# Optimization experiments

Hardware: AMD Instinct MI355X
Metric: run time of the kernel (lower is better)

## Reference

```python
import jax, jax.numpy as jnp
import numpy as np
from jax import lax

H = 64  # hidden size


def _lstm_layer(x, w_ih, w_hh, b_ih, b_hh):
    """Single LSTM layer, batch_first x: [B, T, D] -> [B, T, H].
    PyTorch gate order: i, f, g, o."""
    B = x.shape[0]
    # Precompute input projections for all timesteps: [T, B, 4H]
    xg = jnp.einsum('btd,gd->tbg', x, w_ih) + (b_ih + b_hh)

    def step(carry, xg_t):
        h, c = carry
        gates = xg_t + h @ w_hh.T  # [B, 4H]
        i, f, g, o = jnp.split(gates, 4, axis=-1)
        i = jax.nn.sigmoid(i)
        f = jax.nn.sigmoid(f)
        g = jnp.tanh(g)
        o = jax.nn.sigmoid(o)
        c = f * c + i * g
        h = o * jnp.tanh(c)
        return (h, c), h

    h0 = jnp.zeros((B, H), dtype=x.dtype)
    c0 = jnp.zeros((B, H), dtype=x.dtype)
    (_, _), hs = lax.scan(step, (h0, c0), xg)  # hs: [T, B, H]
    return jnp.swapaxes(hs, 0, 1)  # [B, T, H]


def setup_inputs() -> dict:
    key = jax.random.key(0)
    ks = jax.random.split(key, 11)
    s = 1.0 / np.sqrt(H)  # PyTorch LSTM init scale
    x = jax.random.normal(ks[0], (8192, 168, 7), dtype=jnp.float32)
    return {
        'x': x,
        'w_ih0': jax.random.normal(ks[1], (4 * H, 7), jnp.float32) * s,
        'w_hh0': jax.random.normal(ks[2], (4 * H, H), jnp.float32) * s,
        'b_ih0': jax.random.normal(ks[3], (4 * H,), jnp.float32) * s,
        'b_hh0': jax.random.normal(ks[4], (4 * H,), jnp.float32) * s,
        'w_ih1': jax.random.normal(ks[5], (4 * H, H), jnp.float32) * s,
        'w_hh1': jax.random.normal(ks[6], (4 * H, H), jnp.float32) * s,
        'b_ih1': jax.random.normal(ks[7], (4 * H,), jnp.float32) * s,
        'b_hh1': jax.random.normal(ks[8], (4 * H,), jnp.float32) * s,
        'fc_w': jax.random.normal(ks[9], (4, H), jnp.float32) * s,
        'fc_b': jax.random.normal(ks[10], (4,), jnp.float32) * s,
    }


def reference(x, w_ih0, w_hh0, b_ih0, b_hh0, w_ih1, w_hh1, b_ih1, b_hh1, fc_w, fc_b):
    h1 = _lstm_layer(x, w_ih0, w_hh0, b_ih0, b_hh0)   # [B, T, H]
    h2 = _lstm_layer(h1, w_ih1, w_hh1, b_ih1, b_hh1)  # [B, T, H]
    last = h2[:, -1, :]                               # dropout is identity in eval
    return last @ fc_w.T + fc_b                       # [B, 4]
```

## Files before the change

kernel.cpp:

```cpp
#include <hip/hip_runtime.h>

#define TT 168
#define HH 64
#define DD 7
#define NS 16
#define BB 8192
#define CH 8
#define NTH 1024

typedef float f32x2 __attribute__((ext_vector_type(2)));
typedef float f32x4 __attribute__((ext_vector_type(4)));
typedef _Float16 f16x8 __attribute__((ext_vector_type(8)));

#define MFMA16F(A, B, C) __builtin_amdgcn_mfma_f32_16x16x32_f16((A), (B), (C), 0, 0, 0)

__device__ __forceinline__ f16x8 pack8(f32x4 a, f32x4 b) {
    f16x8 r;
#pragma unroll
    for (int e = 0; e < 4; ++e) { r[e] = (_Float16)a[e]; r[4 + e] = (_Float16)b[e]; }
    return r;
}

__device__ __forceinline__ f32x2 exp2x2(f32x2 a) {
    return (f32x2){__builtin_amdgcn_exp2f(fminf(a.x, 40.0f)),
                   __builtin_amdgcn_exp2f(fminf(a.y, 40.0f))};
}
__device__ __forceinline__ f32x2 rcpx2(f32x2 a) {
    return (f32x2){__builtin_amdgcn_rcpf(a.x), __builtin_amdgcn_rcpf(a.y)};
}

__device__ __forceinline__ void cell_pair(f32x2 si, f32x2 sf, f32x2 sg, f32x2 so,
                                          f32x2& cs, unsigned& dpk) {
    const f32x2 one = {1.0f, 1.0f};
    const f32x2 ui  = exp2x2(si);
    const f32x2 uf  = exp2x2(sf);
    const f32x2 ug  = exp2x2(sg);
    const f32x2 opf = one + uf;
    const f32x2 pig = (one + ui) * (one + ug);
    const f32x2 R1  = rcpx2(pig * opf);
    const f32x2 fv  = pig * R1;
    const f32x2 igs = (ug * 2.88539008f - (f32x2){2.88539008f, 2.88539008f}) * (opf * R1);
    cs = fv * cs + igs;
    const f32x2 uo = exp2x2(so);
    const f32x2 uc = exp2x2(cs);
    const f32x2 R2 = rcpx2((one + uo) * (one + uc));
    const f32x2 hv = (one - uc) * R2;
    asm("v_cvt_pkrtz_f16_f32 %0, %1, %2" : "=v"(dpk) : "v"(hv.x), "v"(hv.y));
}

__global__ __launch_bounds__(NTH, 8)
void weather_lstm_mfma(const float* __restrict__ x,
                       const float* __restrict__ w_ih0, const float* __restrict__ w_hh0,
                       const float* __restrict__ b_ih0, const float* __restrict__ b_hh0,
                       const float* __restrict__ w_ih1, const float* __restrict__ w_hh1,
                       const float* __restrict__ b_ih1, const float* __restrict__ b_hh1,
                       const float* __restrict__ fc_w, const float* __restrict__ fc_b,
                       float* __restrict__ out)
{
    __shared__ f16x8 xs[2][CH][4][NS];
    __shared__ __align__(16) _Float16 h1[2][NS][72];
    __shared__ __align__(16) _Float16 h2[2][NS][72];

    const int tid  = threadIdx.x;
    const int wv   = tid >> 6;
    const int u    = wv & 7;
    const int lane = tid & 63;
    const int col  = lane & 15;
    const int kg   = lane >> 4;
    const int s0   = blockIdx.x * NS;
    const int uw   = 8 * u + 2 * kg;

    for (int i = tid; i < 2 * NS * 72; i += NTH) {
        ((short*)h1)[i] = 0; ((short*)h2)[i] = 0;
    }
    {
        const f16x8 z8i = {0, 0, 0, 0, 0, 0, 0, 0};
        f16x8* xf = &xs[0][0][0][0];
        for (int i = tid; i < 2 * CH * 4 * NS; i += NTH) xf[i] = z8i;
    }
    __syncthreads();
    if (tid < CH * NS) {
        const int tloc = tid >> 4, ss = tid & 15;
        const float* px = x + ((size_t)(s0 + ss) * TT + tloc) * DD;
        f32x4 a, b;
        a[0] = px[0]; a[1] = px[1]; a[2] = px[2]; a[3] = px[3];
        b[0] = px[4]; b[1] = px[5]; b[2] = px[6]; b[3] = 1.0f;
        xs[0][tloc][0][ss] = pack8(a, b);
    }
    __syncthreads();

    const f32x4 zz = {0, 0, 0, 0};

    if (wv < 8) {
        f16x8 W0[2][2], WX[2];
#pragma unroll
        for (int t = 0; t < 2; ++t) {
            const int gsel = 2 * t + (col & 1);
            const float sc = (gsel == 2) ? -2.88539008f : -1.44269504f;
            const int row = 64 * gsel + 8 * u + (col >> 1);
#pragma unroll
            for (int kf = 0; kf < 2; ++kf) {
                const float* p = w_hh0 + (size_t)row * HH + 32 * kf + 8 * kg;
                W0[t][kf] = pack8(*(const f32x4*)p * sc, *(const f32x4*)(p + 4) * sc);
            }
            f32x4 a = {0, 0, 0, 0}, b = {0, 0, 0, 0};
            if (kg == 0) {
                const float* p = w_ih0 + (size_t)row * DD;
                a[0] = p[0]; a[1] = p[1]; a[2] = p[2]; a[3] = p[3];
                b[0] = p[4]; b[1] = p[5]; b[2] = p[6];
                b[3] = b_ih0[row] + b_hh0[row];
            }
            WX[t] = pack8(a * sc, b * sc);
        }
        f32x2 cs = {0, 0};

        const f16x8* xk = &xs[0][0][kg][col];
        const _Float16* r0 = &h1[0][col][8 * kg];
        const _Float16* r1 = r0 + NS * 72;
        unsigned* wp0 = (unsigned*)&h1[0][col][uw];
        unsigned* wp1 = (unsigned*)((_Float16*)wp0 + NS * 72);

        auto l0_step = [&](int xofs, const _Float16* r, unsigned* wr) {
            const f16x8 ax = xk[xofs];
            f32x4 aP = MFMA16F(WX[0], ax, zz);
            f32x4 aQ = MFMA16F(WX[1], ax, zz);
            f16x8 dh = *(const f16x8*)r;
            aP = MFMA16F(W0[0][0], dh, aP);
            aQ = MFMA16F(W0[1][0], dh, aQ);
            dh = *(const f16x8*)(r + 32);
            aP = MFMA16F(W0[0][1], dh, aP);
            aQ = MFMA16F(W0[1][1], dh, aQ);
            unsigned dpk;
            cell_pair((f32x2){aP[0], aP[2]}, (f32x2){aP[1], aP[3]},
                      (f32x2){aQ[0], aQ[2]}, (f32x2){aQ[1], aQ[3]}, cs, dpk);
            *wr = dpk;
        };
        auto refill = [&](int kref) {
            if (tid < CH * NS) {
                const int tloc = tid >> 4, ss = tid & 15;
                const int tg = kref + CH + tloc;
                const float* px = x + ((size_t)(s0 + ss) * TT + tg) * DD;
                f32x4 a, b;
                a[0] = px[0]; a[1] = px[1]; a[2] = px[2]; a[3] = px[3];
                b[0] = px[4]; b[1] = px[5]; b[2] = px[6]; b[3] = 1.0f;
                const int nb = ((kref >> 3) & 1) ^ 1;
                xs[nb][tloc][0][ss] = pack8(a, b);
            }
        };

        refill(0);
        l0_step(0, r1, wp0);
        __syncthreads();
        l0_step(64, r0, wp1);
        __syncthreads();

#pragma unroll 1
        for (int j = 1; j < 84; ++j) {
            const int xofs = ((2 * j) & 15) * 64;
            if ((j & 3) == 0 && j < 80) refill(2 * j);
            l0_step(xofs, r1, wp0);
            __syncthreads();
            l0_step(xofs + 64, r0, wp1);
            __syncthreads();
        }
        __syncthreads();
    } else {
        f16x8 W1[2][4];
        f32x4 bias1[2];
#pragma unroll
        for (int t = 0; t < 2; ++t) {
            const int gsel = 2 * t + (col & 1);
            const float sc = (gsel == 2) ? -2.88539008f : -1.44269504f;
            const int row = 64 * gsel + 8 * u + (col >> 1);
#pragma unroll
            for (int kf = 0; kf < 4; ++kf) {
                const float* base = (kf < 2) ? (w_ih1 + (size_t)row * HH + 32 * kf)
                                             : (w_hh1 + (size_t)row * HH + 32 * (kf - 2));
                const float* p = base + 8 * kg;
                W1[t][kf] = pack8(*(const f32x4*)p * sc, *(const f32x4*)(p + 4) * sc);
            }
#pragma unroll
            for (int e = 0; e < 4; ++e) {
                const int g2 = 2 * t + (e & 1);
                const float sce = (g2 == 2) ? -2.88539008f : -1.44269504f;
                const int br = 64 * g2 + 8 * u + 2 * kg + (e >> 1);
                bias1[t][e] = (b_ih1[br] + b_hh1[br]) * sce;
            }
        }
        f32x2 cs = {0, 0};

        const _Float16* p10 = &h1[0][col][8 * kg];
        const _Float16* p11 = p10 + NS * 72;
        const _Float16* p20 = &h2[0][col][8 * kg];
        const _Float16* p21 = p20 + NS * 72;
        unsigned* q0 = (unsigned*)&h2[0][col][uw];
        unsigned* q1 = (unsigned*)((_Float16*)q0 + NS * 72);

        auto l1_step = [&](const _Float16* h1p, const _Float16* h2p, unsigned* wr) {
            f16x8 dh = *(const f16x8*)h1p;
            f32x4 aP = MFMA16F(W1[0][0], dh, bias1[0]);
            f32x4 aQ = MFMA16F(W1[1][0], dh, bias1[1]);
            dh = *(const f16x8*)(h1p + 32);
            aP = MFMA16F(W1[0][1], dh, aP);
            aQ = MFMA16F(W1[1][1], dh, aQ);
            dh = *(const f16x8*)h2p;
            aP = MFMA16F(W1[0][2], dh, aP);
            aQ = MFMA16F(W1[1][2], dh, aQ);
            dh = *(const f16x8*)(h2p + 32);
            aP = MFMA16F(W1[0][3], dh, aP);
            aQ = MFMA16F(W1[1][3], dh, aQ);
            unsigned dpk;
            cell_pair((f32x2){aP[0], aP[2]}, (f32x2){aP[1], aP[3]},
                      (f32x2){aQ[0], aQ[2]}, (f32x2){aQ[1], aQ[3]}, cs, dpk);
            *wr = dpk;
        };

        __syncthreads();
        l1_step(p10, p21, q0);
        __syncthreads();

#pragma unroll 1
        for (int j = 1; j < 84; ++j) {
            l1_step(p11, p20, q1);
            __syncthreads();
            l1_step(p10, p21, q0);
            __syncthreads();
        }
        l1_step(p11, p20, q1);
        __syncthreads();
    }

    if (tid < NS * 4) {
        const int s = tid >> 2, k = tid & 3;
        float a = fc_b[k];
#pragma unroll
        for (int j = 0; j < HH; ++j)
            a = fmaf((float)h2[1][s][j], fc_w[k * HH + j], a);
        out[(size_t)(s0 + s) * 4 + k] = a;
    }
}

extern "C" void kernel_launch(void* const* d_in, const int* in_sizes, int n_in,
                              void* d_out, int out_size, void* d_ws, size_t ws_size,
                              hipStream_t stream) {
    const float* x     = (const float*)d_in[0];
    const float* w_ih0 = (const float*)d_in[1];
    const float* w_hh0 = (const float*)d_in[2];
    const float* b_ih0 = (const float*)d_in[3];
    const float* b_hh0 = (const float*)d_in[4];
    const float* w_ih1 = (const float*)d_in[5];
    const float* w_hh1 = (const float*)d_in[6];
    const float* b_ih1 = (const float*)d_in[7];
    const float* b_hh1 = (const float*)d_in[8];
    const float* fc_w  = (const float*)d_in[9];
    const float* fc_b  = (const float*)d_in[10];
    float* out = (float*)d_out;

    dim3 grid(BB / NS), block(NTH);
    weather_lstm_mfma<<<grid, block, 0, stream>>>(
        x, w_ih0, w_hh0, b_ih0, b_hh0,
        w_ih1, w_hh1, b_ih1, b_hh1, fc_w, fc_b, out);
}
```

Baseline: 227.1 us.

## Split LSTM steps into MFMA and cell phases, staggering layers across barriers

Each recurrent step is split into a matrix-core phase and an elementwise cell phase, separated by block barriers. The layer-0 and layer-1 wave groups are offset so that one group's MFMA phase lines up with the other group's transcendental cell phase. The aim is to let matrix-core and vector/SFU work from the two layers overlap on the CU. The cost is twice as many __syncthreads per step, and the barrier counts of the two branches must match exactly.

```diff
diff --git a/kernel.cpp b/kernel.cpp
--- a/kernel.cpp
+++ b/kernel.cpp
@@ -113,6 +113,7 @@
             WX[t] = pack8(a * sc, b * sc);
         }
         f32x2 cs = {0, 0};
+        f32x4 aP, aQ;
 
         const f16x8* xk = &xs[0][0][kg][col];
         const _Float16* r0 = &h1[0][col][8 * kg];
@@ -120,16 +121,18 @@
         unsigned* wp0 = (unsigned*)&h1[0][col][uw];
         unsigned* wp1 = (unsigned*)((_Float16*)wp0 + NS * 72);
 
-        auto l0_step = [&](int xofs, const _Float16* r, unsigned* wr) {
+        auto l0_mfma = [&](int xofs, const _Float16* r) {
             const f16x8 ax = xk[xofs];
-            f32x4 aP = MFMA16F(WX[0], ax, zz);
-            f32x4 aQ = MFMA16F(WX[1], ax, zz);
+            aP = MFMA16F(WX[0], ax, zz);
+            aQ = MFMA16F(WX[1], ax, zz);
             f16x8 dh = *(const f16x8*)r;
             aP = MFMA16F(W0[0][0], dh, aP);
             aQ = MFMA16F(W0[1][0], dh, aQ);
             dh = *(const f16x8*)(r + 32);
             aP = MFMA16F(W0[0][1], dh, aP);
             aQ = MFMA16F(W0[1][1], dh, aQ);
+        };
+        auto l0_cell = [&](unsigned* wr) {
             unsigned dpk;
             cell_pair((f32x2){aP[0], aP[2]}, (f32x2){aP[1], aP[3]},
                       (f32x2){aQ[0], aQ[2]}, (f32x2){aQ[1], aQ[3]}, cs, dpk);
@@ -149,21 +152,22 @@
         };
 
         refill(0);
-        l0_step(0, r1, wp0);
-        __syncthreads();
-        l0_step(64, r0, wp1);
-        __syncthreads();
+        l0_mfma(0, r1);        __syncthreads();
+        l0_cell(wp0);          __syncthreads();
+        l0_mfma(64, r0);       __syncthreads();
+        l0_cell(wp1);          __syncthreads();
 
 #pragma unroll 1
         for (int j = 1; j < 84; ++j) {
             const int xofs = ((2 * j) & 15) * 64;
             if ((j & 3) == 0 && j < 80) refill(2 * j);
-            l0_step(xofs, r1, wp0);
-            __syncthreads();
-            l0_step(xofs + 64, r0, wp1);
-            __syncthreads();
-        }
-        __syncthreads();
+            l0_mfma(xofs, r1);       __syncthreads();
+            l0_cell(wp0);            __syncthreads();
+            l0_mfma(xofs + 64, r0);  __syncthreads();
+            l0_cell(wp1);            __syncthreads();
+        }
+        __syncthreads(); __syncthreads();
+        __syncthreads(); __syncthreads();
     } else {
         f16x8 W1[2][4];
         f32x4 bias1[2];
@@ -188,6 +192,7 @@
             }
         }
         f32x2 cs = {0, 0};
+        f32x4 bP, bQ;
 
         const _Float16* p10 = &h1[0][col][8 * kg];
         const _Float16* p11 = p10 + NS * 72;
@@ -196,37 +201,41 @@
         unsigned* q0 = (unsigned*)&h2[0][col][uw];
         unsigned* q1 = (unsigned*)((_Float16*)q0 + NS * 72);
 
-        auto l1_step = [&](const _Float16* h1p, const _Float16* h2p, unsigned* wr) {
+        auto l1_mfma = [&](const _Float16* h1p, const _Float16* h2p) {
             f16x8 dh = *(const f16x8*)h1p;
-            f32x4 aP = MFMA16F(W1[0][0], dh, bias1[0]);
-            f32x4 aQ = MFMA16F(W1[1][0], dh, bias1[1]);
+            bP = MFMA16F(W1[0][0], dh, bias1[0]);
+            bQ = MFMA16F(W1[1][0], dh, bias1[1]);
             dh = *(const f16x8*)(h1p + 32);
-            aP = MFMA16F(W1[0][1], dh, aP);
-            aQ = MFMA16F(W1[1][1], dh, aQ);
+            bP = MFMA16F(W1[0][1], dh, bP);
+            bQ = MFMA16F(W1[1][1], dh, bQ);
             dh = *(const f16x8*)h2p;
-            aP = MFMA16F(W1[0][2], dh, aP);
-            aQ = MFMA16F(W1[1][2], dh, aQ);
+            bP = MFMA16F(W1[0][2], dh, bP);
+            bQ = MFMA16F(W1[1][2], dh, bQ);
             dh = *(const f16x8*)(h2p + 32);
-            aP = MFMA16F(W1[0][3], dh, aP);
-            aQ = MFMA16F(W1[1][3], dh, aQ);
+            bP = MFMA16F(W1[0][3], dh, bP);
+            bQ = MFMA16F(W1[1][3], dh, bQ);
+        };
+        auto l1_cell = [&](unsigned* wr) {
             unsigned dpk;
-            cell_pair((f32x2){aP[0], aP[2]}, (f32x2){aP[1], aP[3]},
-                      (f32x2){aQ[0], aQ[2]}, (f32x2){aQ[1], aQ[3]}, cs, dpk);
+            cell_pair((f32x2){bP[0], bP[2]}, (f32x2){bP[1], bP[3]},
+                      (f32x2){bQ[0], bQ[2]}, (f32x2){bQ[1], bQ[3]}, cs, dpk);
             *wr = dpk;
         };
 
+        __syncthreads(); __syncthreads();
         __syncthreads();
-        l1_step(p10, p21, q0);
-        __syncthreads();
+        l1_mfma(p10, p21);     __syncthreads();
 
 #pragma unroll 1
         for (int j = 1; j < 84; ++j) {
-            l1_step(p11, p20, q1);
-            __syncthreads();
-            l1_step(p10, p21, q0);
-            __syncthreads();
-        }
-        l1_step(p11, p20, q1);
+            l1_cell(q0);          __syncthreads();
+            l1_mfma(p11, p20);    __syncthreads();
+            l1_cell(q1);          __syncthreads();
+            l1_mfma(p10, p21);    __syncthreads();
+        }
+        l1_cell(q0);          __syncthreads();
+        l1_mfma(p11, p20);    __syncthreads();
+        l1_cell(q1);          __syncthreads();
         __syncthreads();
     }
 
```

After: 228.7 us. Within noise of the previous version (+0.7%).
